# Kernel optimization log

Measured on AMD Instinct MI355X. Metric: run time of the kernel, lower is better.

Reference implementation:

```python
import jax, jax.numpy as jnp
import numpy as np

B, N, D, C = 32, 8192, 256, 1000  # batch, nodes, dim (dim_original == dim_attention), num_class


def setup_inputs() -> dict:
    key = jax.random.key(0)
    ks = jax.random.split(key, 6)
    s = 1.0 / np.sqrt(D)
    return {
        "atom": jax.random.normal(ks[0], (B, N, D), dtype=jnp.float32),
        "obj": jax.random.normal(ks[1], (B, D), dtype=jnp.float32),
        "W": jax.random.uniform(ks[2], (D, D), jnp.float32, -s, s),        # nn.Linear(D, D, bias=False).weight
        "A": jax.random.uniform(ks[3], (1, 2 * D), jnp.float32, -1.0 / np.sqrt(2 * D), 1.0 / np.sqrt(2 * D)),  # nn.Linear(2D, 1, bias=False).weight
        "CW": jax.random.uniform(ks[4], (C, 2 * D), jnp.float32, -1.0 / np.sqrt(2 * D), 1.0 / np.sqrt(2 * D)),  # classifier weight
        "CB": jax.random.uniform(ks[5], (C,), jnp.float32, -1.0 / np.sqrt(2 * D), 1.0 / np.sqrt(2 * D)),        # classifier bias
    }


def reference(atom, obj, W, A, CW, CB):
    # a1 = w(atom): [B, N, D]; o1 = w(obj): [B, D]
    a1 = jnp.einsum("bnd,kd->bnk", atom, W)
    o1 = obj @ W.T
    # att = Linear_a(cat(a1, broadcast(o1)))  == a1 @ A1 + o1 @ A2 (no concat materialized)
    A1, A2 = A[0, :D], A[0, D:]
    att = a1 @ A1 + (o1 @ A2)[:, None]          # [B, N] attention scores (no softmax)
    # message_a2o = att_weights.bmm(a1).squeeze(): [B, D]
    msg = jnp.einsum("bn,bnd->bd", att, a1)
    # inte == 'concat': classifier(cat(o1, msg))
    preds = jnp.concatenate([o1, msg], axis=-1) @ CW.T + CB  # [B, C]
    return preds
```

## Files before the change

kernel.cpp:

```cpp
#include <hip/hip_runtime.h>

#define DD 256
#define BB 32
#define NN 8192
#define CC 1000
#define SUBS 64

typedef float f4 __attribute__((ext_vector_type(4)));

__device__ __forceinline__ f4 ntload(const float* p) {
    return __builtin_nontemporal_load((const f4*)p);
}

template <int CTRL>
__device__ __forceinline__ float dpp_ror_add(float s) {
    int r = __builtin_amdgcn_update_dpp(0, __float_as_int(s), CTRL, 0xF, 0xF, true);
    return s + __int_as_float(r);
}
__device__ __forceinline__ float rowsum16(float s) {
    s = dpp_ror_add<0x121>(s);
    s = dpp_ror_add<0x122>(s);
    s = dpp_ror_add<0x124>(s);
    s = dpp_ror_add<0x128>(s);
    return s;
}

__global__ __launch_bounds__(256) void k_v(const float* __restrict__ W,
                                           const float* __restrict__ A,
                                           float* __restrict__ vpart) {
    int i = blockIdx.x, d = threadIdx.x;
    int k0 = i * 16;
    float s1 = 0.f, s2 = 0.f;
#pragma unroll
    for (int k = 0; k < 16; ++k) {
        float w = W[(size_t)(k0 + k) * DD + d];
        s1 += A[k0 + k] * w;
        s2 += A[DD + k0 + k] * w;
    }
    vpart[i * 2 * DD + d]      = s1;
    vpart[i * 2 * DD + DD + d] = s2;
}

__global__ __launch_bounds__(256) void k_c(const float* __restrict__ vpart,
                                           const float* __restrict__ obj,
                                           float* __restrict__ v1,
                                           float* __restrict__ c) {
    int t = threadIdx.x;
    __shared__ float sv2[DD];
    float s1 = 0.f, s2 = 0.f;
#pragma unroll
    for (int i = 0; i < 16; ++i) {
        s1 += vpart[i * 2 * DD + t];
        s2 += vpart[i * 2 * DD + DD + t];
    }
    v1[t]  = s1;
    sv2[t] = s2;
    __syncthreads();
    int wave = t >> 6, lane = t & 63;
    f4 v = *(const f4*)&sv2[lane * 4];
#pragma unroll
    for (int i = 0; i < 8; ++i) {
        int b = wave * 8 + i;
        f4 o = *(const f4*)(obj + (size_t)b * DD + lane * 4);
        float p = o.x * v.x + o.y * v.y + o.z * v.z + o.w * v.w;
        p = rowsum16(p);
        p += __shfl_xor(p, 16, 64);
        p += __shfl_xor(p, 32, 64);
        if (lane == 0) c[b] = p;
    }
}

__global__ __launch_bounds__(256) void k_main(const float* __restrict__ atom,
                                              const float* __restrict__ v1,
                                              const float* __restrict__ c,
                                              float* __restrict__ partials) {
    int blk  = blockIdx.x;
    int b    = blk >> 6;
    int sub  = blk & 63;
    int tid  = threadIdx.x;
    int wave = tid >> 6, lane = tid & 63;
    int grp  = lane >> 4, gl = lane & 15;

    __shared__ float sv1[DD];
    __shared__ float tsh[4][DD];
    sv1[tid] = v1[tid];
    __syncthreads();
    float4 w0 = *(const float4*)&sv1[gl * 4];
    float4 w1 = *(const float4*)&sv1[gl * 4 + 64];
    float4 w2 = *(const float4*)&sv1[gl * 4 + 128];
    float4 w3 = *(const float4*)&sv1[gl * 4 + 192];
    float  cb = c[b];

    const float* base = atom + ((size_t)b * NN + (size_t)sub * 128 + wave * 32 + grp) * DD;

    f4 A0 = {0.f, 0.f, 0.f, 0.f}, A1 = A0, A2 = A0, A3 = A0;

#pragma unroll 4
    for (int g = 0; g < 8; ++g) {
        const float* rp = base + (size_t)g * 4 * DD;
        f4 x0 = ntload(rp + gl * 4);
        f4 x1 = ntload(rp + gl * 4 + 64);
        f4 x2 = ntload(rp + gl * 4 + 128);
        f4 x3 = ntload(rp + gl * 4 + 192);
        float dot = x0.x * w0.x + x0.y * w0.y + x0.z * w0.z + x0.w * w0.w
                  + x1.x * w1.x + x1.y * w1.y + x1.z * w1.z + x1.w * w1.w
                  + x2.x * w2.x + x2.y * w2.y + x2.z * w2.z + x2.w * w2.w
                  + x3.x * w3.x + x3.y * w3.y + x3.z * w3.z + x3.w * w3.w;
        float att = rowsum16(dot) + cb;
        A0 += att * x0;
        A1 += att * x1;
        A2 += att * x2;
        A3 += att * x3;
    }

#define XRED(v)                              \
    v.x += __shfl_xor(v.x, 16, 64); v.x += __shfl_xor(v.x, 32, 64); \
    v.y += __shfl_xor(v.y, 16, 64); v.y += __shfl_xor(v.y, 32, 64); \
    v.z += __shfl_xor(v.z, 16, 64); v.z += __shfl_xor(v.z, 32, 64); \
    v.w += __shfl_xor(v.w, 16, 64); v.w += __shfl_xor(v.w, 32, 64);
    XRED(A0) XRED(A1) XRED(A2) XRED(A3)
#undef XRED

    if (grp == 0) {
        *(f4*)&tsh[wave][gl * 4]       = A0;
        *(f4*)&tsh[wave][gl * 4 + 64]  = A1;
        *(f4*)&tsh[wave][gl * 4 + 128] = A2;
        *(f4*)&tsh[wave][gl * 4 + 192] = A3;
    }
    __syncthreads();
    partials[(size_t)blk * DD + tid] =
        tsh[0][tid] + tsh[1][tid] + tsh[2][tid] + tsh[3][tid];
}

__global__ __launch_bounds__(256) void k_mid(const float* __restrict__ partials,
                                             const float* __restrict__ W,
                                             const float* __restrict__ obj,
                                             float* __restrict__ x) {
    int b = blockIdx.x >> 4, q = blockIdx.x & 15;
    int t = threadIdx.x;
    __shared__ float tt[DD];
    __shared__ float so[DD];

    float s = 0.f;
#pragma unroll 8
    for (int i = 0; i < SUBS; ++i) s += partials[((size_t)(b * SUBS + i)) * DD + t];
    tt[t] = s;
    so[t] = obj[(size_t)b * DD + t];
    __syncthreads();

    int kk = t >> 4, cs = t & 15;
    int k  = q * 16 + kk;
    const float4* wr = (const float4*)(W + (size_t)k * DD + cs * 16);
    const float4* tv = (const float4*)(tt + cs * 16);
    const float4* ov = (const float4*)(so + cs * 16);
    float p = 0.f, po = 0.f;
#pragma unroll
    for (int i = 0; i < 4; ++i) {
        float4 a = wr[i], xx = tv[i], oo = ov[i];
        p  += a.x * xx.x + a.y * xx.y + a.z * xx.z + a.w * xx.w;
        po += a.x * oo.x + a.y * oo.y + a.z * oo.z + a.w * oo.w;
    }
    p  = rowsum16(p);
    po = rowsum16(po);
    if (cs == 0) {
        x[b * 2 * DD + DD + k] = p;
        x[b * 2 * DD + k]      = po;
    }
}

__global__ __launch_bounds__(256) void k_class(const float* __restrict__ x,
                                               const float* __restrict__ CW,
                                               const float* __restrict__ CB,
                                               float* __restrict__ out) {
    int bg = blockIdx.x / 63, ch = blockIdx.x % 63;
    int t = threadIdx.x;
    __shared__ float xs[4][2 * DD];

    {
        const float4* src = (const float4*)(x + (size_t)bg * 4 * 2 * DD);
        float4* dst = (float4*)&xs[0][0];
        dst[t]       = src[t];
        dst[t + 256] = src[t + 256];
    }
    __syncthreads();

    int cl = t >> 4, seg = t & 15;
    int j = ch * 16 + cl;
    if (j < CC) {
        const float4* cw = (const float4*)(CW + (size_t)j * 2 * DD + seg * 32);
        const float4* x0 = (const float4*)(&xs[0][seg * 32]);
        const float4* x1 = (const float4*)(&xs[1][seg * 32]);
        const float4* x2 = (const float4*)(&xs[2][seg * 32]);
        const float4* x3 = (const float4*)(&xs[3][seg * 32]);
        float p0 = 0.f, p1 = 0.f, p2 = 0.f, p3 = 0.f;
#pragma unroll
        for (int i = 0; i < 8; ++i) {
            float4 a = cw[i];
            float4 v0 = x0[i], v1 = x1[i], v2 = x2[i], v3 = x3[i];
            p0 += a.x * v0.x + a.y * v0.y + a.z * v0.z + a.w * v0.w;
            p1 += a.x * v1.x + a.y * v1.y + a.z * v1.z + a.w * v1.w;
            p2 += a.x * v2.x + a.y * v2.y + a.z * v2.z + a.w * v2.w;
            p3 += a.x * v3.x + a.y * v3.y + a.z * v3.z + a.w * v3.w;
        }
        p0 = rowsum16(p0); p1 = rowsum16(p1);
        p2 = rowsum16(p2); p3 = rowsum16(p3);
        if (seg == 0) {
            float cb = CB[j];
            int b0 = bg * 4;
            out[(b0 + 0) * CC + j] = p0 + cb;
            out[(b0 + 1) * CC + j] = p1 + cb;
            out[(b0 + 2) * CC + j] = p2 + cb;
            out[(b0 + 3) * CC + j] = p3 + cb;
        }
    }
}

extern "C" void kernel_launch(void* const* d_in, const int* in_sizes, int n_in,
                              void* d_out, int out_size, void* d_ws, size_t ws_size,
                              hipStream_t stream) {
    const float* atom = (const float*)d_in[0];
    const float* obj  = (const float*)d_in[1];
    const float* W    = (const float*)d_in[2];
    const float* A    = (const float*)d_in[3];
    const float* CW   = (const float*)d_in[4];
    const float* CB   = (const float*)d_in[5];
    float* out = (float*)d_out;

    float* ws = (float*)d_ws;
    float* v1       = ws;
    float* c        = ws + 256;
    float* x        = ws + 512;
    float* vpart    = x + (size_t)BB * 2 * DD;
    float* partials = vpart + 16 * 2 * DD;

    hipLaunchKernelGGL(k_v,     dim3(16),        dim3(256), 0, stream, W, A, vpart);
    hipLaunchKernelGGL(k_c,     dim3(1),         dim3(256), 0, stream, vpart, obj, v1, c);
    hipLaunchKernelGGL(k_main,  dim3(BB * SUBS), dim3(256), 0, stream, atom, v1, c, partials);
    hipLaunchKernelGGL(k_mid,   dim3(BB * 16),   dim3(256), 0, stream, partials, W, obj, x);
    hipLaunchKernelGGL(k_class, dim3(8 * 63),    dim3(256), 0, stream, x, CW, CB, out);
}
```

Measured before the change: 68.74 us.

## Fuse prep kernels, halve main-kernel split, batch 8 rows in classifier

Merges the two small prep kernels (v = W^T A and the per-batch obj bias) into one kernel with 32 blocks, each recomputing v redundantly, which removes a launch and a dependency. The main streaming kernel now processes 256 rows per block with 32 sub-blocks per batch instead of 64, so there are fewer partials for the mid kernel to reduce. The classifier processes 8 batch rows per block so each CW row is reused more, and LDS reads in the mid and classifier kernels are rotated by lane segment to reduce bank conflicts. The trade-offs are less parallelism in the memory-bound main kernel (1024 blocks instead of 2048) and redundant W reads in the prep kernel.

New measurement: 67.25 us. 1.02x faster.

```diff
diff --git a/kernel.cpp b/kernel.cpp
--- a/kernel.cpp
+++ b/kernel.cpp
@@ -4,7 +4,7 @@
 #define BB 32
 #define NN 8192
 #define CC 1000
-#define SUBS 64
+#define SUBS 32
 
 typedef float f4 __attribute__((ext_vector_type(4)));
 
@@ -25,49 +25,36 @@
     return s;
 }
 
-__global__ __launch_bounds__(256) void k_v(const float* __restrict__ W,
-                                           const float* __restrict__ A,
-                                           float* __restrict__ vpart) {
-    int i = blockIdx.x, d = threadIdx.x;
-    int k0 = i * 16;
-    float s1 = 0.f, s2 = 0.f;
-#pragma unroll
-    for (int k = 0; k < 16; ++k) {
-        float w = W[(size_t)(k0 + k) * DD + d];
-        s1 += A[k0 + k] * w;
-        s2 += A[DD + k0 + k] * w;
-    }
-    vpart[i * 2 * DD + d]      = s1;
-    vpart[i * 2 * DD + DD + d] = s2;
-}
-
-__global__ __launch_bounds__(256) void k_c(const float* __restrict__ vpart,
-                                           const float* __restrict__ obj,
-                                           float* __restrict__ v1,
-                                           float* __restrict__ c) {
-    int t = threadIdx.x;
-    __shared__ float sv2[DD];
-    float s1 = 0.f, s2 = 0.f;
-#pragma unroll
-    for (int i = 0; i < 16; ++i) {
-        s1 += vpart[i * 2 * DD + t];
-        s2 += vpart[i * 2 * DD + DD + t];
-    }
-    v1[t]  = s1;
-    sv2[t] = s2;
-    __syncthreads();
-    int wave = t >> 6, lane = t & 63;
-    f4 v = *(const f4*)&sv2[lane * 4];
-#pragma unroll
-    for (int i = 0; i < 8; ++i) {
-        int b = wave * 8 + i;
-        f4 o = *(const f4*)(obj + (size_t)b * DD + lane * 4);
-        float p = o.x * v.x + o.y * v.y + o.z * v.z + o.w * v.w;
-        p = rowsum16(p);
-        p += __shfl_xor(p, 16, 64);
-        p += __shfl_xor(p, 32, 64);
-        if (lane == 0) c[b] = p;
-    }
+__global__ __launch_bounds__(256) void k_prep(const float* __restrict__ W,
+                                              const float* __restrict__ A,
+                                              const float* __restrict__ obj,
+                                              float* __restrict__ v1,
+                                              float* __restrict__ c) {
+    int b = blockIdx.x, t = threadIdx.x;
+    int q  = t >> 6;
+    int cs = (t & 63) * 4;
+    __shared__ float s1[4][DD], s2[4][DD];
+    __shared__ float sc[4];
+    f4 a1 = {0.f, 0.f, 0.f, 0.f}, a2 = a1;
+#pragma unroll 8
+    for (int k = q; k < DD; k += 4) {
+        f4 w = *(const f4*)(W + (size_t)k * DD + cs);
+        a1 += A[k] * w;
+        a2 += A[DD + k] * w;
+    }
+    *(f4*)&s1[q][cs] = a1;
+    *(f4*)&s2[q][cs] = a2;
+    __syncthreads();
+    float vv1 = s1[0][t] + s1[1][t] + s1[2][t] + s1[3][t];
+    float vv2 = s2[0][t] + s2[1][t] + s2[2][t] + s2[3][t];
+    if (b == 0) v1[t] = vv1;
+    float p = vv2 * obj[(size_t)b * DD + t];
+    p = rowsum16(p);
+    p += __shfl_xor(p, 16, 64);
+    p += __shfl_xor(p, 32, 64);
+    if ((t & 63) == 0) sc[t >> 6] = p;
+    __syncthreads();
+    if (t == 0) c[b] = sc[0] + sc[1] + sc[2] + sc[3];
 }
 
 __global__ __launch_bounds__(256) void k_main(const float* __restrict__ atom,
@@ -75,8 +62,8 @@
                                               const float* __restrict__ c,
                                               float* __restrict__ partials) {
     int blk  = blockIdx.x;
-    int b    = blk >> 6;
-    int sub  = blk & 63;
+    int b    = blk >> 5;
+    int sub  = blk & 31;
     int tid  = threadIdx.x;
     int wave = tid >> 6, lane = tid & 63;
     int grp  = lane >> 4, gl = lane & 15;
@@ -91,12 +78,12 @@
     float4 w3 = *(const float4*)&sv1[gl * 4 + 192];
     float  cb = c[b];
 
-    const float* base = atom + ((size_t)b * NN + (size_t)sub * 128 + wave * 32 + grp) * DD;
+    const float* base = atom + ((size_t)b * NN + (size_t)sub * 256 + wave * 64 + grp) * DD;
 
     f4 A0 = {0.f, 0.f, 0.f, 0.f}, A1 = A0, A2 = A0, A3 = A0;
 
 #pragma unroll 4
-    for (int g = 0; g < 8; ++g) {
+    for (int g = 0; g < 16; ++g) {
         const float* rp = base + (size_t)g * 4 * DD;
         f4 x0 = ntload(rp + gl * 4);
         f4 x1 = ntload(rp + gl * 4 + 64);
@@ -151,12 +138,13 @@
     int kk = t >> 4, cs = t & 15;
     int k  = q * 16 + kk;
     const float4* wr = (const float4*)(W + (size_t)k * DD + cs * 16);
-    const float4* tv = (const float4*)(tt + cs * 16);
-    const float4* ov = (const float4*)(so + cs * 16);
     float p = 0.f, po = 0.f;
 #pragma unroll
-    for (int i = 0; i < 4; ++i) {
-        float4 a = wr[i], xx = tv[i], oo = ov[i];
+    for (int ii = 0; ii < 4; ++ii) {
+        int i = (ii + cs) & 3;
+        float4 a  = wr[i];
+        float4 xx = *(const float4*)&tt[cs * 16 + i * 4];
+        float4 oo = *(const float4*)&so[cs * 16 + i * 4];
         p  += a.x * xx.x + a.y * xx.y + a.z * xx.z + a.w * xx.w;
         po += a.x * oo.x + a.y * oo.y + a.z * oo.z + a.w * oo.w;
     }
@@ -174,43 +162,41 @@
                                                float* __restrict__ out) {
     int bg = blockIdx.x / 63, ch = blockIdx.x % 63;
     int t = threadIdx.x;
-    __shared__ float xs[4][2 * DD];
+    __shared__ float xs[8][2 * DD];
 
     {
-        const float4* src = (const float4*)(x + (size_t)bg * 4 * 2 * DD);
-        float4* dst = (float4*)&xs[0][0];
-        dst[t]       = src[t];
-        dst[t + 256] = src[t + 256];
+        const f4* src = (const f4*)(x + (size_t)bg * 8 * 2 * DD);
+        f4* dst = (f4*)&xs[0][0];
+#pragma unroll
+        for (int i = 0; i < 4; ++i) dst[t + 256 * i] = src[t + 256 * i];
     }
     __syncthreads();
 
     int cl = t >> 4, seg = t & 15;
     int j = ch * 16 + cl;
     if (j < CC) {
-        const float4* cw = (const float4*)(CW + (size_t)j * 2 * DD + seg * 32);
-        const float4* x0 = (const float4*)(&xs[0][seg * 32]);
-        const float4* x1 = (const float4*)(&xs[1][seg * 32]);
-        const float4* x2 = (const float4*)(&xs[2][seg * 32]);
-        const float4* x3 = (const float4*)(&xs[3][seg * 32]);
-        float p0 = 0.f, p1 = 0.f, p2 = 0.f, p3 = 0.f;
-#pragma unroll
-        for (int i = 0; i < 8; ++i) {
-            float4 a = cw[i];
-            float4 v0 = x0[i], v1 = x1[i], v2 = x2[i], v3 = x3[i];
-            p0 += a.x * v0.x + a.y * v0.y + a.z * v0.z + a.w * v0.w;
-            p1 += a.x * v1.x + a.y * v1.y + a.z * v1.z + a.w * v1.w;
-            p2 += a.x * v2.x + a.y * v2.y + a.z * v2.z + a.w * v2.w;
-            p3 += a.x * v3.x + a.y * v3.y + a.z * v3.z + a.w * v3.w;
+        const f4* cw = (const f4*)(CW + (size_t)j * 2 * DD + seg * 32);
+        float p[8];
+#pragma unroll
+        for (int bb = 0; bb < 8; ++bb) p[bb] = 0.f;
+#pragma unroll
+        for (int ii = 0; ii < 8; ++ii) {
+            int i = (ii + seg) & 7;
+            f4 a = cw[i];
+#pragma unroll
+            for (int bb = 0; bb < 8; ++bb) {
+                f4 v = *(const f4*)&xs[bb][seg * 32 + i * 4];
+                p[bb] += a.x * v.x + a.y * v.y + a.z * v.z + a.w * v.w;
+            }
         }
-        p0 = rowsum16(p0); p1 = rowsum16(p1);
-        p2 = rowsum16(p2); p3 = rowsum16(p3);
+#pragma unroll
+        for (int bb = 0; bb < 8; ++bb) p[bb] = rowsum16(p[bb]);
         if (seg == 0) {
             float cb = CB[j];
-            int b0 = bg * 4;
-            out[(b0 + 0) * CC + j] = p0 + cb;
-            out[(b0 + 1) * CC + j] = p1 + cb;
-            out[(b0 + 2) * CC + j] = p2 + cb;
-            out[(b0 + 3) * CC + j] = p3 + cb;
+            int b0 = bg * 8;
+#pragma unroll
+            for (int bb = 0; bb < 8; ++bb)
+                out[(size_t)(b0 + bb) * CC + j] = p[bb] + cb;
         }
     }
 }
@@ -230,12 +216,10 @@
     float* v1       = ws;
     float* c        = ws + 256;
     float* x        = ws + 512;
-    float* vpart    = x + (size_t)BB * 2 * DD;
-    float* partials = vpart + 16 * 2 * DD;
-
-    hipLaunchKernelGGL(k_v,     dim3(16),        dim3(256), 0, stream, W, A, vpart);
-    hipLaunchKernelGGL(k_c,     dim3(1),         dim3(256), 0, stream, vpart, obj, v1, c);
+    float* partials = x + (size_t)BB * 2 * DD;
+
+    hipLaunchKernelGGL(k_prep,  dim3(BB),        dim3(256), 0, stream, W, A, obj, v1, c);
     hipLaunchKernelGGL(k_main,  dim3(BB * SUBS), dim3(256), 0, stream, atom, v1, c, partials);
     hipLaunchKernelGGL(k_mid,   dim3(BB * 16),   dim3(256), 0, stream, partials, W, obj, x);
-    hipLaunchKernelGGL(k_class, dim3(8 * 63),    dim3(256), 0, stream, x, CW, CB, out);
-}
+    hipLaunchKernelGGL(k_class, dim3(4 * 63),    dim3(256), 0, stream, x, CW, CB, out);
+}
```
